# Kernel optimization log

Hardware: AMD Instinct MI355X
Metric: run time of the kernel (lower is better)

Reference implementation:

```python
import jax, jax.numpy as jnp
import numpy as np

B, S, H2 = 32, 4096, 512  # H2 = 2*hidden_size


def setup_inputs() -> dict:
    key = jax.random.key(0)
    ks = jax.random.split(key, 10)
    s = 1.0 / np.sqrt(H2)
    return {
        "decoder_state": jax.random.normal(ks[0], (B, 1, H2), jnp.float32),
        "encoder_outputs": jax.random.normal(ks[1], (B, S, H2), jnp.float32),
        "coverage_vector": jax.random.uniform(ks[2], (B, S, H2), jnp.float32),
        "W_h": jax.random.uniform(ks[3], (H2, H2), jnp.float32, -s, s),
        "b_h": jax.random.uniform(ks[4], (H2,), jnp.float32, -s, s),
        "W_s": jax.random.uniform(ks[5], (H2, H2), jnp.float32, -s, s),
        "b_s": jax.random.uniform(ks[6], (H2,), jnp.float32, -s, s),
        "W_c": jax.random.uniform(ks[7], (H2, H2), jnp.float32, -s, s),
        "b_c": jax.random.uniform(ks[8], (H2,), jnp.float32, -s, s),
        "v": jax.random.uniform(ks[9], (H2, 1), jnp.float32, -s, s),
    }


def reference(decoder_state, encoder_outputs, coverage_vector,
              W_h, b_h, W_s, b_s, W_c, b_c, v):
    # additive attention features: [B, S, 2H]
    e = jnp.tanh(encoder_outputs @ W_h + b_h
                 + decoder_state @ W_s + b_s      # broadcasts over S
                 + coverage_vector @ W_c + b_c)
    scores = e @ v                                # [B, S, 1]
    attn_dist = jax.nn.softmax(scores, axis=1)    # softmax over source positions
    # weighted sum of encoder outputs: [B, 1, 2H]
    h_star_t = jnp.einsum('bsi,bsd->bid', attn_dist, encoder_outputs)
    coverage_new = coverage_vector + attn_dist    # broadcast over feature dim
    return h_star_t, attn_dist, coverage_new
```

## Files before the change

kernel.cpp:

```cpp
#include <hip/hip_runtime.h>
#include <hip/hip_bf16.h>
#include <stdint.h>

#define H2    512
#define BATCH 32
#define SEQ   4096
#define BM    64
#define BK    64
#define NKT   16

typedef __attribute__((ext_vector_type(4))) float f32x4;
typedef __attribute__((ext_vector_type(8))) short bf16x8;

__device__ __forceinline__ unsigned short f2bf(float f) {
    union { float f; unsigned u; } v; v.f = f;
    unsigned r = v.u + 0x7FFF + ((v.u >> 16) & 1);
    return (unsigned short)(r >> 16);
}

__device__ __forceinline__ float fast_tanh(float x) {
    float e = __builtin_amdgcn_exp2f(x * 2.88539008177793f);
    return 1.0f - 2.0f * __builtin_amdgcn_rcpf(e + 1.0f);
}

__global__ void kprep_w(const float* __restrict__ Wh, const float* __restrict__ Wc,
                        unsigned short* __restrict__ wt) {
    int c    = blockIdx.x * blockDim.x + threadIdx.x;
    int lane = c & 63;
    int cb   = (c >> 6) & 31;
    int ks   = (c >> 11) & 1;
    int kt   = c >> 12;
    int col  = cb * 16 + (lane & 15);
    int k0   = kt * 64 + ks * 32 + (lane >> 4) * 8;
    unsigned short tmp[8];
#pragma unroll
    for (int j = 0; j < 8; ++j) {
        int kg = k0 + j;
        float w = (kg < 512) ? Wh[kg * 512 + col] : Wc[(kg - 512) * 512 + col];
        tmp[j] = f2bf(w);
    }
    *reinterpret_cast<uint4*>(wt + (size_t)c * 8) = *reinterpret_cast<const uint4*>(tmp);
}

__global__ void kprep_q(const float* __restrict__ dec, const float* __restrict__ Ws,
                        const float* __restrict__ bh, const float* __restrict__ bs,
                        const float* __restrict__ bc, float* __restrict__ q) {
    __shared__ float dsh[512];
    int b = blockIdx.x, t = threadIdx.x;
    dsh[t]       = dec[b * 512 + t];
    dsh[t + 256] = dec[b * 512 + 256 + t];
    __syncthreads();
    float a0 = 0.f, a1 = 0.f;
#pragma unroll 4
    for (int k = 0; k < 512; ++k) {
        float d = dsh[k];
        a0 = fmaf(d, Ws[k * 512 + t], a0);
        a1 = fmaf(d, Ws[k * 512 + 256 + t], a1);
    }
    q[b * 512 + t]       = a0 + bh[t] + bs[t] + bc[t];
    q[b * 512 + 256 + t] = a1 + bh[256 + t] + bs[256 + t] + bc[256 + t];
}

__launch_bounds__(512, 2)
__global__ void kgemm(const float* __restrict__ enc, const float* __restrict__ cov,
                      const unsigned short* __restrict__ wt,
                      const float* __restrict__ q, const float* __restrict__ vvec,
                      float* __restrict__ scores) {
    __shared__ unsigned short Asm[2][BM * BK];
    __shared__ float qv[H2];
    __shared__ float vv[H2];
    __shared__ float sred[BM][8];

    int tid  = threadIdx.x;
    int lane = tid & 63, wn = tid >> 6;

    int cpx  = gridDim.x >> 3;
    int swz  = (blockIdx.x & 7) * cpx + (blockIdx.x >> 3);
    int row0 = swz * BM;

    qv[tid] = q[(row0 >> 12) * H2 + tid];
    vv[tid] = vvec[tid];

    int r = tid >> 3, k8 = tid & 7;
    const float* ae = enc + (size_t)(row0 + r) * H2 + k8 * 8;
    const float* ac = cov + (size_t)(row0 + r) * H2 + k8 * 8;
    unsigned awb = (unsigned)(r * 128 + ((k8 * 16) ^ ((r & 7) << 4)));

    unsigned arb[2];
    arb[0] = (unsigned)((lane & 15) * 128 +
             ((((lane >> 4) << 4))        ^ ((lane & 7) << 4)));
    arb[1] = (unsigned)((lane & 15) * 128 +
             (((64 + ((lane >> 4) << 4))) ^ ((lane & 7) << 4)));

    const bf16x8* bb = reinterpret_cast<const bf16x8*>(wt) + (size_t)wn * 4 * 64 + lane;

    f32x4  acc[4][4] = {};
    bf16x8 bfr[2][2][4];
    f32x4  pA[2][2];

#pragma unroll
    for (int ks = 0; ks < 2; ++ks)
#pragma unroll
        for (int ni = 0; ni < 4; ++ni)
            bfr[0][ks][ni] = bb[ks * 2048 + ni * 64];
    {
        f32x4 a0 = *reinterpret_cast<const f32x4*>(ae);
        f32x4 a1 = *reinterpret_cast<const f32x4*>(ae + 4);
        pA[0][0] = *reinterpret_cast<const f32x4*>(ae + 64);
        pA[0][1] = *reinterpret_cast<const f32x4*>(ae + 68);
        union { unsigned short h[8]; uint4 u; } t;
#pragma unroll
        for (int j = 0; j < 4; ++j) { t.h[j] = f2bf(a0[j]); t.h[4 + j] = f2bf(a1[j]); }
        *reinterpret_cast<uint4*>((char*)Asm[0] + awb) = t.u;
    }
    asm volatile("s_waitcnt lgkmcnt(0)" ::: "memory");
    __builtin_amdgcn_sched_barrier(0);
    __builtin_amdgcn_s_barrier();
    __builtin_amdgcn_sched_barrier(0);

#pragma unroll
    for (int kt = 0; kt < NKT; ++kt) {
        const int cur = kt & 1, nxt = cur ^ 1;
        bf16x8 af[2][4];
#pragma unroll
        for (int ks = 0; ks < 2; ++ks)
#pragma unroll
            for (int mi = 0; mi < 4; ++mi)
                af[ks][mi] = *reinterpret_cast<const bf16x8*>(
                    (const char*)Asm[cur] + mi * 2048 + arb[ks]);
        if (kt + 1 < NKT) {
#pragma unroll
            for (int ks = 0; ks < 2; ++ks)
#pragma unroll
                for (int ni = 0; ni < 4; ++ni)
                    bfr[nxt][ks][ni] = bb[(size_t)((kt + 1) * 2 + ks) * 2048 + ni * 64];
        }
        if (kt + 2 < NKT) {
            const float* src = (kt + 2 < 8) ? (ae + (kt + 2) * 64) : (ac + (kt - 6) * 64);
            pA[nxt][0] = *reinterpret_cast<const f32x4*>(src);
            pA[nxt][1] = *reinterpret_cast<const f32x4*>(src + 4);
        }
        __builtin_amdgcn_sched_barrier(0);
        __builtin_amdgcn_s_setprio(1);
#pragma unroll
        for (int ks = 0; ks < 2; ++ks)
#pragma unroll
            for (int mi = 0; mi < 4; ++mi)
#pragma unroll
                for (int ni = 0; ni < 4; ++ni)
                    acc[mi][ni] = __builtin_amdgcn_mfma_f32_16x16x32_bf16(
                        af[ks][mi], bfr[cur][ks][ni], acc[mi][ni], 0, 0, 0);
        __builtin_amdgcn_s_setprio(0);
        if (kt + 1 < NKT) {
            union { unsigned short h[8]; uint4 u; } t;
#pragma unroll
            for (int j = 0; j < 4; ++j) {
                t.h[j]     = f2bf(pA[cur][0][j]);
                t.h[4 + j] = f2bf(pA[cur][1][j]);
            }
            *reinterpret_cast<uint4*>((char*)Asm[nxt] + awb) = t.u;
        }
        asm volatile("s_waitcnt lgkmcnt(0)" ::: "memory");
        __builtin_amdgcn_sched_barrier(0);
        __builtin_amdgcn_s_barrier();
        __builtin_amdgcn_sched_barrier(0);
    }

    float ps[4][4] = {};
#pragma unroll
    for (int mi = 0; mi < 4; ++mi)
#pragma unroll
        for (int ni = 0; ni < 4; ++ni) {
            int colg = wn * 64 + ni * 16 + (lane & 15);
            float qq = qv[colg], vl = vv[colg];
#pragma unroll
            for (int j = 0; j < 4; ++j) {
                float e = fast_tanh(acc[mi][ni][j] + qq);
                ps[mi][j] = fmaf(e, vl, ps[mi][j]);
            }
        }
#pragma unroll
    for (int mi = 0; mi < 4; ++mi)
#pragma unroll
        for (int j = 0; j < 4; ++j) {
            float s = ps[mi][j];
            s += __shfl_xor(s, 1);
            s += __shfl_xor(s, 2);
            s += __shfl_xor(s, 4);
            s += __shfl_xor(s, 8);
            if ((lane & 15) == 0)
                sred[mi * 16 + (lane >> 4) * 4 + j][wn] = s;
        }
    __syncthreads();
    if (tid < BM) {
        float s = 0.f;
#pragma unroll
        for (int w = 0; w < 8; ++w) s += sred[tid][w];
        scores[row0 + tid] = s;
    }
}

__global__ void ksoftmax(const float* __restrict__ scores, float* __restrict__ out) {
    __shared__ float redm[16];
    __shared__ float reds[16];
    int b = blockIdx.x, t = threadIdx.x, lane = t & 63, w = t >> 6;
    if (t < 512) out[b * 512 + t] = 0.0f;
    f32x4 sv = *reinterpret_cast<const f32x4*>(scores + b * 4096 + t * 4);
    float m = fmaxf(fmaxf(sv[0], sv[1]), fmaxf(sv[2], sv[3]));
#pragma unroll
    for (int o = 1; o < 64; o <<= 1) m = fmaxf(m, __shfl_xor(m, o));
    if (lane == 0) redm[w] = m;
    __syncthreads();
    float mm = redm[0];
#pragma unroll
    for (int i = 1; i < 16; ++i) mm = fmaxf(mm, redm[i]);

    f32x4 p;
#pragma unroll
    for (int j = 0; j < 4; ++j)
        p[j] = __builtin_amdgcn_exp2f((sv[j] - mm) * 1.4426950408889634f);
    float s = p[0] + p[1] + p[2] + p[3];
#pragma unroll
    for (int o = 1; o < 64; o <<= 1) s += __shfl_xor(s, o);
    if (lane == 0) reds[w] = s;
    __syncthreads();
    float tot = 0.f;
#pragma unroll
    for (int i = 0; i < 16; ++i) tot += reds[i];
    float rinv = __builtin_amdgcn_rcpf(tot);
    p *= rinv;
    *reinterpret_cast<f32x4*>(out + 16384 + b * 4096 + t * 4) = p;
}

__global__ void kcov(const float* __restrict__ enc, const float* __restrict__ cov,
                     float* __restrict__ out) {
    const float* attn = out + 16384;
    float* covn  = out + 16384 + 131072;
    float* hstar = out;
    int blk = blockIdx.x;
    int b = blk >> 6, ck = blk & 63;
    int s0 = ck * 64;
    int t  = threadIdx.x;
    int f4 = (t & 127) * 4;
    int rp = t >> 7;
    size_t base = (size_t)b * SEQ * H2;
    f32x4 h = {0.f, 0.f, 0.f, 0.f};
#pragma unroll 2
    for (int i = 0; i < 32; ++i) {
        int s = s0 + i * 2 + rp;
        float a = attn[b * 4096 + s];
        size_t idx = base + (size_t)s * H2 + f4;
        f32x4 e4 = *reinterpret_cast<const f32x4*>(enc + idx);
        f32x4 c4 = *reinterpret_cast<const f32x4*>(cov + idx);
        c4 += a;
        __builtin_nontemporal_store(c4, reinterpret_cast<f32x4*>(covn + idx));
        h += a * e4;
    }
    int off = b * 512 + f4;
    atomicAdd(&hstar[off + 0], h[0]);
    atomicAdd(&hstar[off + 1], h[1]);
    atomicAdd(&hstar[off + 2], h[2]);
    atomicAdd(&hstar[off + 3], h[3]);
}

extern "C" void kernel_launch(void* const* d_in, const int* in_sizes, int n_in,
                              void* d_out, int out_size, void* d_ws, size_t ws_size,
                              hipStream_t stream) {
    const float* dec = (const float*)d_in[0];
    const float* enc = (const float*)d_in[1];
    const float* cov = (const float*)d_in[2];
    const float* Wh  = (const float*)d_in[3];
    const float* bh  = (const float*)d_in[4];
    const float* Ws  = (const float*)d_in[5];
    const float* bs  = (const float*)d_in[6];
    const float* Wc  = (const float*)d_in[7];
    const float* bc  = (const float*)d_in[8];
    const float* v   = (const float*)d_in[9];
    float* out = (float*)d_out;

    char* ws = (char*)d_ws;
    unsigned short* wt = (unsigned short*)ws;
    float* q      = (float*)(ws + (1 << 20));
    float* scores = (float*)(ws + (1 << 20) + 65536);

    kprep_w <<<dim3(256),  dim3(256),  0, stream>>>(Wh, Wc, wt);
    kprep_q <<<dim3(32),   dim3(256),  0, stream>>>(dec, Ws, bh, bs, bc, q);
    kgemm   <<<dim3(2048), dim3(512),  0, stream>>>(enc, cov, wt, q, v, scores);
    ksoftmax<<<dim3(32),   dim3(1024), 0, stream>>>(scores, out);
    kcov    <<<dim3(2048), dim3(256),  0, stream>>>(enc, cov, out);
}
```

Before: 411.8 us.

## Shrink GEMM K-tile to 32, halve register buffers, raise occupancy to four blocks

The fused score GEMM now steps through K in 32-wide tiles (32 steps) instead of 64-wide ones, so it keeps only one set of B fragments and smaller A prefetch registers. This lets launch bounds request four blocks per CU instead of two. The weight prep layout, the LDS swizzle and the tile size are changed to match, and the f32-to-bf16 conversion now uses packed v_cvt_pk_bf16_f32 instructions. Loading the q and v vectors is moved after the main loop, behind an explicit sync. The trade-off is twice as many barriers, and the B loads for the next step are issued right after the MFMAs, which gives less time to hide their latency.

```diff
diff --git a/kernel.cpp b/kernel.cpp
--- a/kernel.cpp
+++ b/kernel.cpp
@@ -6,8 +6,7 @@
 #define BATCH 32
 #define SEQ   4096
 #define BM    64
-#define BK    64
-#define NKT   16
+#define NKT3  32
 
 typedef __attribute__((ext_vector_type(4))) float f32x4;
 typedef __attribute__((ext_vector_type(8))) short bf16x8;
@@ -16,6 +15,13 @@
     union { float f; unsigned u; } v; v.f = f;
     unsigned r = v.u + 0x7FFF + ((v.u >> 16) & 1);
     return (unsigned short)(r >> 16);
+}
+
+__device__ __forceinline__ uint2 cvt4_bf16(f32x4 a) {
+    uint2 r;
+    asm("v_cvt_pk_bf16_f32 %0, %1, %2" : "=v"(r.x) : "v"(a[0]), "v"(a[1]));
+    asm("v_cvt_pk_bf16_f32 %0, %1, %2" : "=v"(r.y) : "v"(a[2]), "v"(a[3]));
+    return r;
 }
 
 __device__ __forceinline__ float fast_tanh(float x) {
@@ -28,10 +34,9 @@
     int c    = blockIdx.x * blockDim.x + threadIdx.x;
     int lane = c & 63;
     int cb   = (c >> 6) & 31;
-    int ks   = (c >> 11) & 1;
-    int kt   = c >> 12;
+    int kt   = c >> 11;
     int col  = cb * 16 + (lane & 15);
-    int k0   = kt * 64 + ks * 32 + (lane >> 4) * 8;
+    int k0   = kt * 32 + (lane >> 4) * 8;
     unsigned short tmp[8];
 #pragma unroll
     for (int j = 0; j < 8; ++j) {
@@ -61,12 +66,12 @@
     q[b * 512 + 256 + t] = a1 + bh[256 + t] + bs[256 + t] + bc[256 + t];
 }
 
-__launch_bounds__(512, 2)
+__launch_bounds__(512, 4)
 __global__ void kgemm(const float* __restrict__ enc, const float* __restrict__ cov,
                       const unsigned short* __restrict__ wt,
                       const float* __restrict__ q, const float* __restrict__ vvec,
                       float* __restrict__ scores) {
-    __shared__ unsigned short Asm[2][BM * BK];
+    __shared__ unsigned short Asm[2][2048];
     __shared__ float qv[H2];
     __shared__ float vv[H2];
     __shared__ float sred[BM][8];
@@ -78,93 +83,118 @@
     int swz  = (blockIdx.x & 7) * cpx + (blockIdx.x >> 3);
     int row0 = swz * BM;
 
-    qv[tid] = q[(row0 >> 12) * H2 + tid];
-    vv[tid] = vvec[tid];
-
-    int r = tid >> 3, k8 = tid & 7;
-    const float* ae = enc + (size_t)(row0 + r) * H2 + k8 * 8;
-    const float* ac = cov + (size_t)(row0 + r) * H2 + k8 * 8;
-    unsigned awb = (unsigned)(r * 128 + ((k8 * 16) ^ ((r & 7) << 4)));
-
-    unsigned arb[2];
-    arb[0] = (unsigned)((lane & 15) * 128 +
-             ((((lane >> 4) << 4))        ^ ((lane & 7) << 4)));
-    arb[1] = (unsigned)((lane & 15) * 128 +
-             (((64 + ((lane >> 4) << 4))) ^ ((lane & 7) << 4)));
-
-    const bf16x8* bb = reinterpret_cast<const bf16x8*>(wt) + (size_t)wn * 4 * 64 + lane;
+    int r = tid >> 3, k4 = tid & 7;
+    const float* aeb = enc + (size_t)(row0 + r) * H2 + k4 * 4;
+    const float* acb = cov + (size_t)(row0 + r) * H2 + k4 * 4;
+    unsigned awb = (unsigned)((r >> 4) * 1024 + (k4 >> 1) * 256 +
+                              (((r & 15) * 16) ^ ((k4 >> 1) << 4)) + (k4 & 1) * 8);
+    unsigned arb = (unsigned)((lane >> 4) * 256 +
+                              (((lane & 15) * 16) ^ ((lane >> 4) << 4)));
+    const unsigned short* bbase = wt + ((size_t)(wn * 4) * 64 + lane) * 8;
 
     f32x4  acc[4][4] = {};
-    bf16x8 bfr[2][2][4];
-    f32x4  pA[2][2];
-
-#pragma unroll
-    for (int ks = 0; ks < 2; ++ks)
-#pragma unroll
-        for (int ni = 0; ni < 4; ++ni)
-            bfr[0][ks][ni] = bb[ks * 2048 + ni * 64];
+    bf16x8 bfr[4];
+    f32x4  pA[2];
+
+#define A_SRC(T) (((T) < 16) ? (aeb + (T) * 32) : (acb + ((T) - 16) * 32))
+
+#pragma unroll
+    for (int ni = 0; ni < 4; ++ni)
+        bfr[ni] = *reinterpret_cast<const bf16x8*>(bbase + ni * 512);
+    f32x4 a0 = *reinterpret_cast<const f32x4*>(A_SRC(0));
+    pA[1]    = *reinterpret_cast<const f32x4*>(A_SRC(1));
+    __builtin_amdgcn_sched_barrier(0);
     {
-        f32x4 a0 = *reinterpret_cast<const f32x4*>(ae);
-        f32x4 a1 = *reinterpret_cast<const f32x4*>(ae + 4);
-        pA[0][0] = *reinterpret_cast<const f32x4*>(ae + 64);
-        pA[0][1] = *reinterpret_cast<const f32x4*>(ae + 68);
-        union { unsigned short h[8]; uint4 u; } t;
-#pragma unroll
-        for (int j = 0; j < 4; ++j) { t.h[j] = f2bf(a0[j]); t.h[4 + j] = f2bf(a1[j]); }
-        *reinterpret_cast<uint4*>((char*)Asm[0] + awb) = t.u;
+        uint2 u = cvt4_bf16(a0);
+        *reinterpret_cast<uint2*>((char*)Asm[0] + awb) = u;
     }
     asm volatile("s_waitcnt lgkmcnt(0)" ::: "memory");
     __builtin_amdgcn_sched_barrier(0);
     __builtin_amdgcn_s_barrier();
     __builtin_amdgcn_sched_barrier(0);
 
-#pragma unroll
-    for (int kt = 0; kt < NKT; ++kt) {
-        const int cur = kt & 1, nxt = cur ^ 1;
-        bf16x8 af[2][4];
-#pragma unroll
-        for (int ks = 0; ks < 2; ++ks)
-#pragma unroll
-            for (int mi = 0; mi < 4; ++mi)
-                af[ks][mi] = *reinterpret_cast<const bf16x8*>(
-                    (const char*)Asm[cur] + mi * 2048 + arb[ks]);
-        if (kt + 1 < NKT) {
-#pragma unroll
-            for (int ks = 0; ks < 2; ++ks)
-#pragma unroll
-                for (int ni = 0; ni < 4; ++ni)
-                    bfr[nxt][ks][ni] = bb[(size_t)((kt + 1) * 2 + ks) * 2048 + ni * 64];
-        }
-        if (kt + 2 < NKT) {
-            const float* src = (kt + 2 < 8) ? (ae + (kt + 2) * 64) : (ac + (kt - 6) * 64);
-            pA[nxt][0] = *reinterpret_cast<const f32x4*>(src);
-            pA[nxt][1] = *reinterpret_cast<const f32x4*>(src + 4);
-        }
-        __builtin_amdgcn_sched_barrier(0);
+#pragma unroll 2
+    for (int t = 0; t < NKT3 - 2; ++t) {
+        const int cur = t & 1, nxt = cur ^ 1;
+        bf16x8 af[4];
+#pragma unroll
+        for (int mi = 0; mi < 4; ++mi)
+            af[mi] = *reinterpret_cast<const bf16x8*>(
+                (char*)Asm[cur] + mi * 1024 + arb);
         __builtin_amdgcn_s_setprio(1);
 #pragma unroll
-        for (int ks = 0; ks < 2; ++ks)
-#pragma unroll
-            for (int mi = 0; mi < 4; ++mi)
-#pragma unroll
-                for (int ni = 0; ni < 4; ++ni)
-                    acc[mi][ni] = __builtin_amdgcn_mfma_f32_16x16x32_bf16(
-                        af[ks][mi], bfr[cur][ks][ni], acc[mi][ni], 0, 0, 0);
+        for (int mi = 0; mi < 4; ++mi)
+#pragma unroll
+            for (int ni = 0; ni < 4; ++ni)
+                acc[mi][ni] = __builtin_amdgcn_mfma_f32_16x16x32_bf16(
+                    af[mi], bfr[ni], acc[mi][ni], 0, 0, 0);
         __builtin_amdgcn_s_setprio(0);
-        if (kt + 1 < NKT) {
-            union { unsigned short h[8]; uint4 u; } t;
-#pragma unroll
-            for (int j = 0; j < 4; ++j) {
-                t.h[j]     = f2bf(pA[cur][0][j]);
-                t.h[4 + j] = f2bf(pA[cur][1][j]);
-            }
-            *reinterpret_cast<uint4*>((char*)Asm[nxt] + awb) = t.u;
+        __builtin_amdgcn_sched_barrier(0);
+#pragma unroll
+        for (int ni = 0; ni < 4; ++ni)
+            bfr[ni] = *reinterpret_cast<const bf16x8*>(
+                bbase + (size_t)(t + 1) * 16384 + ni * 512);
+        pA[cur] = *reinterpret_cast<const f32x4*>(A_SRC(t + 2));
+        __builtin_amdgcn_sched_barrier(0);
+        {
+            uint2 u = cvt4_bf16(pA[nxt]);
+            *reinterpret_cast<uint2*>((char*)Asm[nxt] + awb) = u;
         }
         asm volatile("s_waitcnt lgkmcnt(0)" ::: "memory");
         __builtin_amdgcn_sched_barrier(0);
         __builtin_amdgcn_s_barrier();
         __builtin_amdgcn_sched_barrier(0);
     }
+
+    {
+        bf16x8 af[4];
+#pragma unroll
+        for (int mi = 0; mi < 4; ++mi)
+            af[mi] = *reinterpret_cast<const bf16x8*>(
+                (char*)Asm[0] + mi * 1024 + arb);
+        __builtin_amdgcn_s_setprio(1);
+#pragma unroll
+        for (int mi = 0; mi < 4; ++mi)
+#pragma unroll
+            for (int ni = 0; ni < 4; ++ni)
+                acc[mi][ni] = __builtin_amdgcn_mfma_f32_16x16x32_bf16(
+                    af[mi], bfr[ni], acc[mi][ni], 0, 0, 0);
+        __builtin_amdgcn_s_setprio(0);
+        __builtin_amdgcn_sched_barrier(0);
+#pragma unroll
+        for (int ni = 0; ni < 4; ++ni)
+            bfr[ni] = *reinterpret_cast<const bf16x8*>(
+                bbase + (size_t)31 * 16384 + ni * 512);
+        __builtin_amdgcn_sched_barrier(0);
+        {
+            uint2 u = cvt4_bf16(pA[1]);
+            *reinterpret_cast<uint2*>((char*)Asm[1] + awb) = u;
+        }
+        asm volatile("s_waitcnt lgkmcnt(0)" ::: "memory");
+        __builtin_amdgcn_sched_barrier(0);
+        __builtin_amdgcn_s_barrier();
+        __builtin_amdgcn_sched_barrier(0);
+    }
+    {
+        bf16x8 af[4];
+#pragma unroll
+        for (int mi = 0; mi < 4; ++mi)
+            af[mi] = *reinterpret_cast<const bf16x8*>(
+                (char*)Asm[1] + mi * 1024 + arb);
+        __builtin_amdgcn_s_setprio(1);
+#pragma unroll
+        for (int mi = 0; mi < 4; ++mi)
+#pragma unroll
+            for (int ni = 0; ni < 4; ++ni)
+                acc[mi][ni] = __builtin_amdgcn_mfma_f32_16x16x32_bf16(
+                    af[mi], bfr[ni], acc[mi][ni], 0, 0, 0);
+        __builtin_amdgcn_s_setprio(0);
+    }
+#undef A_SRC
+
+    qv[tid] = q[(row0 >> 12) * H2 + tid];
+    vv[tid] = vvec[tid];
+    __syncthreads();
 
     float ps[4][4] = {};
 #pragma unroll
```

Result: faster. 395.7 us (-3.9%).
